# Performance work log

Measured on AMD Instinct MI355X. Metric: run time of the kernel, lower is better.

## Reference

```python
import jax, jax.numpy as jnp
import numpy as np

N, E, F_IN, F_HID, F_OUT, B = 50000, 800000, 128, 128, 128, 64
EPS = 1e-5


def _sage_conv(x, src, dst, w_l, b_l, w_r):
    # PyG SAGEConv (mean aggr): out = lin_l(mean_{j in N(i)} x_j) + lin_r(x_i)
    msg_sum = jax.ops.segment_sum(x[src], dst, num_segments=N)          # [N, F]
    deg = jax.ops.segment_sum(jnp.ones((src.shape[0],), x.dtype), dst, num_segments=N)
    agg = msg_sum / jnp.clip(deg, 1.0)[:, None]
    return agg @ w_l + b_l + x @ w_r


def _batch_norm(x, gamma, beta):
    # PyG BatchNorm (training): biased batch stats over the node dimension
    mu = jnp.mean(x, axis=0)
    var = jnp.mean((x - mu) ** 2, axis=0)
    return (x - mu) * jax.lax.rsqrt(var + EPS) * gamma + beta


def setup_inputs() -> dict:
    key = jax.random.key(0)
    ks = jax.random.split(key, 12)
    x = jax.random.normal(ks[0], (N, F_IN), jnp.float32)
    edge_index = jax.random.randint(ks[1], (2, E), 0, N, jnp.int64 if jax.config.jax_enable_x64 else jnp.int32)
    batch = jnp.sort(jax.random.randint(ks[2], (N,), 0, B))
    s1 = 1.0 / np.sqrt(F_IN)
    s2 = 1.0 / np.sqrt(F_HID)
    return {
        "x": x, "edge_index": edge_index, "batch": batch,
        "w_l1": jax.random.uniform(ks[3], (F_IN, F_HID), jnp.float32, -s1, s1),
        "b_l1": jax.random.uniform(ks[4], (F_HID,), jnp.float32, -s1, s1),
        "w_r1": jax.random.uniform(ks[5], (F_IN, F_HID), jnp.float32, -s1, s1),
        "g1": jnp.ones((F_HID,), jnp.float32),
        "beta1": jnp.zeros((F_HID,), jnp.float32),
        "w_l2": jax.random.uniform(ks[6], (F_HID, F_OUT), jnp.float32, -s2, s2),
        "b_l2": jax.random.uniform(ks[7], (F_OUT,), jnp.float32, -s2, s2),
        "w_r2": jax.random.uniform(ks[8], (F_HID, F_OUT), jnp.float32, -s2, s2),
        "g2": jnp.ones((F_OUT,), jnp.float32),
        "beta2": jnp.zeros((F_OUT,), jnp.float32),
    }


def reference(x, edge_index, batch, w_l1, b_l1, w_r1, g1, beta1, w_l2, b_l2, w_r2, g2, beta2):
    src, dst = edge_index[0], edge_index[1]
    h = jax.nn.relu(_batch_norm(_sage_conv(x, src, dst, w_l1, b_l1, w_r1), g1, beta1))
    h = jax.nn.relu(_batch_norm(_sage_conv(h, src, dst, w_l2, b_l2, w_r2), g2, beta2))
    # global_mean_pool over graph ids
    pooled = jax.ops.segment_sum(h, batch, num_segments=B)              # [B, F_OUT]
    cnt = jax.ops.segment_sum(jnp.ones((N,), h.dtype), batch, num_segments=B)
    return pooled / jnp.clip(cnt, 1.0)[:, None]
```

## Files before the change

kernel.cpp:

```cpp
#include <hip/hip_runtime.h>
#include <hip/hip_bf16.h>
#include <stdint.h>

typedef unsigned int uint32;
typedef unsigned short ushort16;

typedef __attribute__((ext_vector_type(8))) short short8;
typedef __attribute__((ext_vector_type(4))) float f32x4;

#define N_NODES 50000
#define N_EDGES 800000
#define FD      128
#define NGRAPH  64
#define MTILES  3125
#define NBK     196
#define GB      391
#define GB2     782
#define PCH     32
#define KCH     98

__device__ __forceinline__ float bf2f(ushort16 u){
  union { uint32 i; float f; } v; v.i = ((uint32)u) << 16; return v.f;
}
__device__ __forceinline__ float bf2f_lo(uint32 w){ union{uint32 i;float f;}v; v.i = w << 16; return v.f; }
__device__ __forceinline__ float bf2f_hi(uint32 w){ union{uint32 i;float f;}v; v.i = w & 0xffff0000u; return v.f; }
__device__ __forceinline__ ushort16 f2bf(float f){
  uint32 u = __float_as_uint(f);
  u += 0x7fffu + ((u >> 16) & 1u);
  return (ushort16)(u >> 16);
}

__device__ __forceinline__ int ld_idx(const void* p, uint32 is64, size_t i){
  return is64 ? (int)((const long long*)p)[i] : ((const int*)p)[i];
}
__device__ __forceinline__ float ld_f(const void* p, uint32 isf32, int i){
  return isf32 ? ((const float*)p)[i] : bf2f(((const ushort16*)p)[i]);
}

__device__ __forceinline__ void get_flags(const uint32* __restrict__ xw,
    const uint32* __restrict__ eiw, uint32& isf32, uint32& is64)
{
  int l = threadIdx.x & 63;
  uint32 w = xw[l];
  uint32 e8 = (w >> 7) & 0xFFu;
  bool bf_like = (e8 >= 0x70u && e8 <= 0x82u);
  unsigned long long m = __ballot(bf_like);
  isf32 = (__popcll(m) < 32) ? 1u : 0u;
  uint32 hi = (l < 8) ? eiw[2*l + 1] : 1u;
  unsigned long long z = __ballot(hi == 0u);
  is64 = ((z & 0xFFull) == 0xFFull) ? 1u : 0u;
}


__global__ __launch_bounds__(256) void pack_gseg_prep_kernel(
    const void* __restrict__ ei, const void* __restrict__ batch,
    const void* __restrict__ X,
    const void* __restrict__ WL1, const void* __restrict__ WR1,
    const void* __restrict__ WL2, const void* __restrict__ WR2,
    uint32* __restrict__ pack0, uint32* __restrict__ hist, uint32* __restrict__ gstart,
    ushort16* __restrict__ xb, short* __restrict__ wfrag)
{
  uint32 isf32, is64;
  get_flags((const uint32*)X, (const uint32*)ei, isf32, is64);
  int tid = threadIdx.x;
  if (blockIdx.x < GB){
    __shared__ uint32 h[256];
    h[tid] = 0u;
    __syncthreads();
    int base = blockIdx.x*2048;
    for (int r = 0; r < 8; ++r){
      int i = base + r*256 + tid;
      if (i < N_EDGES){
        uint32 s = (uint32)ld_idx(ei, is64, i);
        uint32 d = (uint32)ld_idx(ei, is64, (size_t)N_EDGES + i);
        pack0[i] = (d << 16) | s;
        atomicAdd(&h[d >> 8], 1u);
      }
    }
    __syncthreads();
    hist[blockIdx.x*256 + tid] = h[tid];
  } else if (blockIdx.x < GB + 196){
    int t = (blockIdx.x - GB)*256 + tid;
    if (t >= N_NODES) return;
    int b1 = ld_idx(batch, is64, t);
    int b0 = (t == 0) ? -1 : ld_idx(batch, is64, t - 1);
    for (int g = b0 + 1; g <= b1; ++g) gstart[g] = (uint32)t;
    if (t == N_NODES - 1)
      for (int g = b1 + 1; g <= NGRAPH; ++g) gstart[g] = (uint32)N_NODES;
  } else if (blockIdx.x < GB + 196 + 3125){
    if (!isf32) return;
    size_t e = ((size_t)(blockIdx.x - GB - 196)*256 + tid)*8;
    const float* p = (const float*)X + e;
    float4 u = *(const float4*)p;
    float4 v = *(const float4*)(p + 4);
    uint4 o;
    o.x = (uint32)f2bf(u.x) | ((uint32)f2bf(u.y) << 16);
    o.y = (uint32)f2bf(u.z) | ((uint32)f2bf(u.w) << 16);
    o.z = (uint32)f2bf(v.x) | ((uint32)f2bf(v.y) << 16);
    o.w = (uint32)f2bf(v.z) | ((uint32)f2bf(v.w) << 16);
    *(uint4*)(xb + e) = o;
  } else {
    int t = (blockIdx.x - GB - 196 - 3125)*256 + tid;
    int layer = t >> 15;
    int r = t & 32767;
    int k = r >> 7, n = r & 127;
    const void* w = layer ? (k < 128 ? WL2 : WR2) : (k < 128 ? WL1 : WR1);
    int kk = k & 127;
    float wv = ld_f(w, isf32, kk*128 + n);
    int off = (((k >> 5)*8 + (n >> 4))*64 + (n & 15) + 16*((kk >> 3) & 3))*8 + (kk & 7);
    wfrag[layer*32768 + off] = (short)f2bf(wv);
  }
}

__global__ __launch_bounds__(1024) void scan_hist_kernel(const uint32* __restrict__ hist,
    uint32* __restrict__ off, uint32* __restrict__ bbase)
{
  __shared__ uint32 part[4][256];
  __shared__ uint32 lds[256];
  __shared__ uint32 bb[256];
  int tid = threadIdx.x;
  int seg = tid >> 8, b = tid & 255;
  int k0 = seg*KCH, k1 = (k0 + KCH < GB) ? k0 + KCH : GB;
  uint32 sum = 0;
  for (int k = k0; k < k1; ++k) sum += hist[k*256 + b];
  part[seg][b] = sum;
  __syncthreads();
  uint32 tot = 0, x = 0;
  if (seg == 0){
    tot = part[0][b] + part[1][b] + part[2][b] + part[3][b];
    x = tot; lds[b] = x;
  }
  __syncthreads();
  for (int o = 1; o < 256; o <<= 1){
    uint32 y = 0;
    if (seg == 0 && b >= o) y = lds[b - o];
    __syncthreads();
    if (seg == 0){ x += y; lds[b] = x; }
    __syncthreads();
  }
  if (seg == 0){
    uint32 base = x - tot;
    bb[b] = base;
    if (b <= NBK) bbase[b] = (b < NBK) ? base : (uint32)N_EDGES;
  }
  __syncthreads();
  uint32 run = bb[b];
  for (int s = 0; s < seg; ++s) run += part[s][b];
  for (int k = k0; k < k1; ++k){
    off[k*256 + b] = run;
    run += hist[k*256 + b];
  }
}

__global__ __launch_bounds__(256) void scatter_kernel(const uint32* __restrict__ pack0,
    const uint32* __restrict__ off, uint32* __restrict__ pack1)
{
  __shared__ uint32 cur[256];
  int tid = threadIdx.x;
  cur[tid] = off[blockIdx.x*256 + tid];
  __syncthreads();
  int base = blockIdx.x*2048;
  for (int r = 0; r < 8; ++r){
    int i = base + r*256 + tid;
    if (i < N_EDGES){
      uint32 p = pack0[i];
      uint32 pos = atomicAdd(&cur[p >> 24], 1u);
      pack1[pos] = p;
    }
  }
}

__global__ __launch_bounds__(256) void bucket_csr_kernel(const uint32* __restrict__ pack1,
    const uint32* __restrict__ bbase, uint32* __restrict__ rowstart,
    uint32* __restrict__ deg, ushort16* __restrict__ colidx, uint32* __restrict__ perm)
{
  __shared__ uint32 cnt[256];
  __shared__ uint32 lds[256];
  __shared__ uint32 cur[256];
  __shared__ uint32 dh[64];
  __shared__ uint32 dcur[64];
  int tid = threadIdx.x;
  int bk = blockIdx.x;
  uint32 e0 = bbase[bk], e1 = bbase[bk + 1];
  cnt[tid] = 0u;
  if (tid < 64) dh[tid] = 0u;
  __syncthreads();
  for (uint32 i = e0 + tid; i < e1; i += 256)
    atomicAdd(&cnt[(pack1[i] >> 16) & 255u], 1u);
  __syncthreads();
  uint32 v = cnt[tid];
  uint32 x = v;
  lds[tid] = x; __syncthreads();
  for (int o = 1; o < 256; o <<= 1){
    uint32 y = (tid >= o) ? lds[tid - o] : 0u;
    __syncthreads();
    x += y; lds[tid] = x;
    __syncthreads();
  }
  uint32 start = e0 + x - v;
  int node = bk*256 + tid;
  bool nvalid = node < N_NODES;
  if (nvalid){ rowstart[node] = start; deg[node] = v; }
  cur[tid] = start;
  uint32 bin = (v < 63u) ? v : 63u;
  if (nvalid) atomicAdd(&dh[bin], 1u);
  __syncthreads();
  for (uint32 i = e0 + tid; i < e1; i += 256){
    uint32 p = pack1[i];
    uint32 pos = atomicAdd(&cur[(p >> 16) & 255u], 1u);
    colidx[pos] = (ushort16)(p & 0xFFFFu);
  }
  if (tid == 0){
    uint32 run = 0;
#pragma unroll
    for (int b2 = 0; b2 < 64; ++b2){ dcur[b2] = run; run += dh[b2]; }
  }
  __syncthreads();
  if (nvalid){
    uint32 rank = atomicAdd(&dcur[bin], 1u);
    perm[bk*256 + rank] = (uint32)node;
  }
}


__device__ __forceinline__ void acc8(float* a, uint4 v, const float* s0, const float* h0, int APPLY){
  float f[8];
  f[0] = bf2f_lo(v.x); f[1] = bf2f_hi(v.x);
  f[2] = bf2f_lo(v.y); f[3] = bf2f_hi(v.y);
  f[4] = bf2f_lo(v.z); f[5] = bf2f_hi(v.z);
  f[6] = bf2f_lo(v.w); f[7] = bf2f_hi(v.w);
#pragma unroll
  for (int j = 0; j < 8; ++j)
    a[j] += APPLY ? fmaxf(f[j]*s0[j] + h0[j], 0.f) : f[j];
}

template<int APPLY>
__global__ __launch_bounds__(256) void agg_kernel(const ushort16* __restrict__ Xd,
    const void* __restrict__ Xraw, const void* __restrict__ eiraw,
    const uint32* __restrict__ rowstart, const uint32* __restrict__ deg,
    const ushort16* __restrict__ colidx, const uint32* __restrict__ perm,
    const float* __restrict__ sc, const float* __restrict__ sh,
    ushort16* __restrict__ out)
{
  uint32 isf32, is64;
  get_flags((const uint32*)Xraw, (const uint32*)eiraw, isf32, is64);
  const ushort16* X = (APPLY == 0 && !isf32) ? (const ushort16*)Xraw : Xd;
  int t = blockIdx.x*256 + threadIdx.x;
  int node = (int)perm[t >> 4];
  int l = t & 15;
  uint32 st = rowstart[node];
  uint32 d  = deg[node];
  float s0[8], h0[8];
#pragma unroll
  for (int j = 0; j < 8; ++j){
    s0[j] = APPLY ? sc[l*8 + j] : 0.f;
    h0[j] = APPLY ? sh[l*8 + j] : 0.f;
  }
  float a[8];
#pragma unroll
  for (int j = 0; j < 8; ++j) a[j] = 0.f;
  const ushort16* Xl = X + l*8;
  uint32 i = 0;
  for (; i < d && ((st + i) & 3u); ++i){
    uint32 c = colidx[st + i];
    acc8(a, *(const uint4*)(Xl + (size_t)c*FD), s0, h0, APPLY);
  }
  for (; i + 8 <= d; i += 8){
    uint2 cA = *(const uint2*)(colidx + st + i);
    uint2 cB = *(const uint2*)(colidx + st + i + 4);
    uint4 v0 = *(const uint4*)(Xl + (size_t)(cA.x & 0xFFFFu)*FD);
    uint4 v1 = *(const uint4*)(Xl + (size_t)(cA.x >> 16)*FD);
    uint4 v2 = *(const uint4*)(Xl + (size_t)(cA.y & 0xFFFFu)*FD);
    uint4 v3 = *(const uint4*)(Xl + (size_t)(cA.y >> 16)*FD);
    uint4 v4 = *(const uint4*)(Xl + (size_t)(cB.x & 0xFFFFu)*FD);
    uint4 v5 = *(const uint4*)(Xl + (size_t)(cB.x >> 16)*FD);
    uint4 v6 = *(const uint4*)(Xl + (size_t)(cB.y & 0xFFFFu)*FD);
    uint4 v7 = *(const uint4*)(Xl + (size_t)(cB.y >> 16)*FD);
    acc8(a, v0, s0, h0, APPLY); acc8(a, v1, s0, h0, APPLY);
    acc8(a, v2, s0, h0, APPLY); acc8(a, v3, s0, h0, APPLY);
    acc8(a, v4, s0, h0, APPLY); acc8(a, v5, s0, h0, APPLY);
    acc8(a, v6, s0, h0, APPLY); acc8(a, v7, s0, h0, APPLY);
  }
  for (; i + 4 <= d; i += 4){
    uint2 cA = *(const uint2*)(colidx + st + i);
    uint4 v0 = *(const uint4*)(Xl + (size_t)(cA.x & 0xFFFFu)*FD);
    uint4 v1 = *(const uint4*)(Xl + (size_t)(cA.x >> 16)*FD);
    uint4 v2 = *(const uint4*)(Xl + (size_t)(cA.y & 0xFFFFu)*FD);
    uint4 v3 = *(const uint4*)(Xl + (size_t)(cA.y >> 16)*FD);
    acc8(a, v0, s0, h0, APPLY); acc8(a, v1, s0, h0, APPLY);
    acc8(a, v2, s0, h0, APPLY); acc8(a, v3, s0, h0, APPLY);
  }
  for (; i < d; ++i){
    uint32 c = colidx[st + i];
    acc8(a, *(const uint4*)(Xl + (size_t)c*FD), s0, h0, APPLY);
  }
  float inv = 1.f / fmaxf((float)d, 1.f);
  uint4 o;
  o.x = (uint32)f2bf(a[0]*inv) | ((uint32)f2bf(a[1]*inv) << 16);
  o.y = (uint32)f2bf(a[2]*inv) | ((uint32)f2bf(a[3]*inv) << 16);
  o.z = (uint32)f2bf(a[4]*inv) | ((uint32)f2bf(a[5]*inv) << 16);
  o.w = (uint32)f2bf(a[6]*inv) | ((uint32)f2bf(a[7]*inv) << 16);
  *(uint4*)(out + (size_t)node*FD + l*8) = o;
}


__device__ __forceinline__ short8 affine_relu8(short8 a, const float* sc, const float* sh, int koff){
  short8 r;
#pragma unroll
  for (int j = 0; j < 8; ++j){
    float v = bf2f((ushort16)a[j]) * sc[koff + j] + sh[koff + j];
    r[j] = (short)f2bf(fmaxf(v, 0.f));
  }
  return r;
}

template<int APPLY>
__global__ __launch_bounds__(256) void gemm_bn_kernel(
    const ushort16* __restrict__ A0, const ushort16* __restrict__ A1d,
    const void* __restrict__ A1raw, const void* __restrict__ eiraw,
    const short* __restrict__ wfrag, const void* __restrict__ bias,
    const float* __restrict__ sc, const float* __restrict__ sh,
    const void* __restrict__ Xraw,
    ushort16* __restrict__ hpre, float* __restrict__ bnpart)
{
  __shared__ float red[256];
  uint32 isf32, is64;
  get_flags((const uint32*)Xraw, (const uint32*)eiraw, isf32, is64);
  const ushort16* A1 = (A1raw && !isf32) ? (const ushort16*)A1raw : A1d;
  int tid = threadIdx.x;
  red[tid] = 0.f;
  int wave = tid >> 6, lane = tid & 63, lq = lane >> 4, lm = lane & 15;
  int mt = blockIdx.x*4 + wave;
  bool valid = mt < MTILES;
  size_t m0 = (size_t)((valid ? mt : 0)*16 + lm);
  f32x4 acc[8];
#pragma unroll
  for (int i = 0; i < 8; ++i) acc[i] = (f32x4){0.f,0.f,0.f,0.f};

#pragma unroll
  for (int ks = 0; ks < 8; ++ks){
    int koff = (ks & 3)*32 + lq*8;
    const short* srcp = (const short*)(ks < 4 ? A0 : A1);
    short8 a = *(const short8*)(srcp + m0*FD + koff);
    if (APPLY && ks >= 4) a = affine_relu8(a, sc, sh, koff);
#pragma unroll
    for (int nt = 0; nt < 8; ++nt){
      short8 b = *(const short8*)&wfrag[((ks*8 + nt)*64 + lane)*8];
      acc[nt] = __builtin_amdgcn_mfma_f32_16x16x32_bf16(a, b, acc[nt], 0, 0, 0);
    }
  }

  __syncthreads();
#pragma unroll
  for (int nt = 0; nt < 8; ++nt){
    int colc = nt*16 + lm;
    float bb = ld_f(bias, isf32, colc);
    float s = 0.f, s2 = 0.f;
    if (valid){
      size_t nb = (size_t)mt*16 + lq*4;
#pragma unroll
      for (int r = 0; r < 4; ++r){
        float val = acc[nt][r] + bb;
        hpre[(nb + r)*FD + colc] = f2bf(val);
        s += val; s2 += val*val;
      }
    }
    s  += __shfl_xor(s, 16);  s  += __shfl_xor(s, 32);
    s2 += __shfl_xor(s2, 16); s2 += __shfl_xor(s2, 32);
    if (lq == 0){
      atomicAdd(&red[colc], s);
      atomicAdd(&red[128 + colc], s2);
    }
  }
  __syncthreads();
  bnpart[blockIdx.x*256 + tid] = red[tid];
}


__global__ __launch_bounds__(256) void bn_final_kernel(const float* __restrict__ bnpart,
    const void* __restrict__ gamma, const void* __restrict__ beta,
    const void* __restrict__ Xraw, const void* __restrict__ eiraw,
    float* __restrict__ scale, float* __restrict__ shift)
{
  uint32 isf32, is64;
  get_flags((const uint32*)Xraw, (const uint32*)eiraw, isf32, is64);
  int tid = threadIdx.x;
  int f = blockIdx.x*8 + (tid >> 5);
  int l = tid & 31;
  float s = 0.f, q = 0.f;
  for (int b = l; b < GB2; b += 32){
    s += bnpart[b*256 + f];
    q += bnpart[b*256 + 128 + f];
  }
#pragma unroll
  for (int m = 16; m >= 1; m >>= 1){
    s += __shfl_xor(s, m);
    q += __shfl_xor(q, m);
  }
  if (l == 0){
    const float invN = 1.0f / (float)N_NODES;
    float mu  = s * invN;
    float var = q * invN - mu*mu;
    float scv = ld_f(gamma, isf32, f) * rsqrtf(var + 1e-5f);
    scale[f] = scv;
    shift[f] = ld_f(beta, isf32, f) - mu * scv;
  }
}


__global__ __launch_bounds__(256) void pool_partial_kernel(const ushort16* __restrict__ hp,
    const float* __restrict__ scale, const float* __restrict__ shift,
    const uint32* __restrict__ gstart, float* __restrict__ pool_part)
{
  __shared__ float wred[4*16*8];
  int tid = threadIdx.x;
  int g = blockIdx.x >> 5, chunk = blockIdx.x & 31;
  int slot = tid >> 4, l = tid & 15;
  int wave = tid >> 6, lane = tid & 63;
  uint32 st = gstart[g], cnt = gstart[g+1] - st;
  uint32 per = (cnt + PCH - 1) >> 5;
  uint32 b0 = st + chunk*per;
  uint32 b1 = b0 + per;
  uint32 e1 = st + cnt;
  if (b1 > e1) b1 = e1;
  float s0[8], h0[8], a[8];
#pragma unroll
  for (int j = 0; j < 8; ++j){ s0[j] = scale[l*8 + j]; h0[j] = shift[l*8 + j]; a[j] = 0.f; }
  for (uint32 n = b0 + slot; n < b1; n += 16){
    const uint4 v = *(const uint4*)(hp + (size_t)n*FD + l*8);
    float f[8];
    f[0] = bf2f_lo(v.x); f[1] = bf2f_hi(v.x);
    f[2] = bf2f_lo(v.y); f[3] = bf2f_hi(v.y);
    f[4] = bf2f_lo(v.z); f[5] = bf2f_hi(v.z);
    f[6] = bf2f_lo(v.w); f[7] = bf2f_hi(v.w);
#pragma unroll
    for (int j = 0; j < 8; ++j) a[j] += fmaxf(f[j]*s0[j] + h0[j], 0.f);
  }
#pragma unroll
  for (int j = 0; j < 8; ++j){
    a[j] += __shfl_xor(a[j], 16);
    a[j] += __shfl_xor(a[j], 32);
  }
  if (lane < 16){
#pragma unroll
    for (int j = 0; j < 8; ++j) wred[(wave*16 + lane)*8 + j] = a[j];
  }
  __syncthreads();
  if (tid < 16){
    float r[8];
#pragma unroll
    for (int j = 0; j < 8; ++j)
      r[j] = wred[(0*16 + tid)*8 + j] + wred[(1*16 + tid)*8 + j]
           + wred[(2*16 + tid)*8 + j] + wred[(3*16 + tid)*8 + j];
    float* dst = pool_part + (size_t)blockIdx.x*FD + tid*8;
#pragma unroll
    for (int j = 0; j < 8; ++j) dst[j] = r[j];
  }
}

__global__ void pool_final_kernel(const float* __restrict__ pool_part,
    const uint32* __restrict__ gstart, const void* __restrict__ Xraw,
    const void* __restrict__ eiraw, void* __restrict__ out)
{
  uint32 isf32, is64;
  get_flags((const uint32*)Xraw, (const uint32*)eiraw, isf32, is64);
  int t = blockIdx.x*256 + threadIdx.x;
  int g = t >> 7, f = t & 127;
  float c = fmaxf((float)(gstart[g+1] - gstart[g]), 1.f);
  float v = 0.f;
#pragma unroll 8
  for (int ch = 0; ch < PCH; ++ch)
    v += pool_part[(size_t)(g*PCH + ch)*FD + f];
  v /= c;
  if (isf32) ((float*)out)[t] = v;
  else       ((ushort16*)out)[t] = f2bf(v);
}


extern "C" void kernel_launch(void* const* d_in, const int* in_sizes, int n_in,
                              void* d_out, int out_size, void* d_ws, size_t ws_size,
                              hipStream_t stream)
{
  const void* x   = d_in[0];
  const void* ei  = d_in[1];
  const void* bat = d_in[2];
  const void* wl1 = d_in[3];
  const void* bl1 = d_in[4];
  const void* wr1 = d_in[5];
  const void* g1  = d_in[6];
  const void* be1 = d_in[7];
  const void* wl2 = d_in[8];
  const void* bl2 = d_in[9];
  const void* wr2 = d_in[10];
  const void* g2  = d_in[11];
  const void* be2 = d_in[12];
  char* ws = (char*)d_ws;

  uint32* gstart  = (uint32*)(ws + 64);
  uint32* bbase   = (uint32*)(ws + 384);
  float*  scale1  = (float*) (ws + 1280);
  float*  shift1  = (float*) (ws + 1792);
  float*  scale2  = (float*) (ws + 2304);
  float*  shift2  = (float*) (ws + 2816);
  uint32* rowstart= (uint32*)(ws + 3328);
  uint32* deg     = (uint32*)(ws + 203328);
  ushort16* colidx= (ushort16*)(ws + 403328);
  uint32* perm    = (uint32*)(ws + 2003328);
  short*  wfrag   = (short*) (ws + 2204032);
  float*  bnpart  = (float*) (ws + 2335104);
  ushort16* xb    = (ushort16*)(ws + 3135872);
  ushort16* aggb  = (ushort16*)(ws + 15935872);
  ushort16* hp1   = (ushort16*)(ws + 28735872);
  ushort16* hp2   = (ushort16*)(ws + 41535872);
  uint32* pack0   = (uint32*)(ws + 28735872);
  uint32* pack1   = (uint32*)(ws + 31935872);
  uint32* hist    = (uint32*)(ws + 35135872);
  uint32* off     = (uint32*)(ws + 35536256);
  float*  ppart   = (float*) (ws + 28735872);

  pack_gseg_prep_kernel<<<GB + 196 + 3125 + 256, 256, 0, stream>>>(
      ei, bat, x, wl1, wr1, wl2, wr2, pack0, hist, gstart, xb, wfrag);
  scan_hist_kernel <<<1,  1024, 0, stream>>>(hist, off, bbase);
  scatter_kernel   <<<GB,  256, 0, stream>>>(pack0, off, pack1);
  bucket_csr_kernel<<<NBK, 256, 0, stream>>>(pack1, bbase, rowstart, deg, colidx, perm);

  agg_kernel<0>    <<<3125, 256, 0, stream>>>(xb, x, ei, rowstart, deg, colidx, perm,
                                              nullptr, nullptr, aggb);
  gemm_bn_kernel<0><<<GB2,  256, 0, stream>>>(aggb, xb, x, ei, wfrag, bl1,
                                              nullptr, nullptr, x, hp1, bnpart);
  bn_final_kernel  <<<16,   256, 0, stream>>>(bnpart, g1, be1, x, ei, scale1, shift1);

  agg_kernel<1>    <<<3125, 256, 0, stream>>>(hp1, x, ei, rowstart, deg, colidx, perm,
                                              scale1, shift1, aggb);
  gemm_bn_kernel<1><<<GB2,  256, 0, stream>>>(aggb, hp1, nullptr, ei, wfrag + 32768, bl2,
                                              scale1, shift1, x, hp2, bnpart);
  bn_final_kernel  <<<16,   256, 0, stream>>>(bnpart, g2, be2, x, ei, scale2, shift2);

  pool_partial_kernel<<<NGRAPH*PCH, 256, 0, stream>>>(hp2, scale2, shift2, gstart, ppart);
  pool_final_kernel  <<<32,  256, 0, stream>>>(ppart, gstart, x, ei, d_out);
}
```

Baseline: 297.1 us.

## Split histogram scan into three parallel kernels and drop degree-sorted node permutation

The single-block 1024-thread prefix scan over the edge bucket histogram is replaced by a three-stage scan: partial sums over 16 blocks, a single-block middle scan, and a 16-block offset write. This spreads the serial column walk across more compute units at the cost of two extra launches. Separately, the per-bucket degree-sorting permutation is removed, so the aggregation kernels process nodes in natural order. That saves the perm build and the indirection load, but gives up degree-balanced wavefronts, which may increase divergence in the gather loops.

```diff
diff --git a/kernel.cpp b/kernel.cpp
--- a/kernel.cpp
+++ b/kernel.cpp
@@ -17,7 +17,8 @@
 #define GB      391
 #define GB2     782
 #define PCH     32
-#define KCH     98
+#define SBK     16
+#define KCH2    25
 
 __device__ __forceinline__ float bf2f(ushort16 u){
   union { uint32 i; float f; } v; v.i = ((uint32)u) << 16; return v.f;
@@ -112,40 +113,49 @@
   }
 }
 
-__global__ __launch_bounds__(1024) void scan_hist_kernel(const uint32* __restrict__ hist,
-    uint32* __restrict__ off, uint32* __restrict__ bbase)
-{
-  __shared__ uint32 part[4][256];
-  __shared__ uint32 lds[256];
-  __shared__ uint32 bb[256];
-  int tid = threadIdx.x;
-  int seg = tid >> 8, b = tid & 255;
-  int k0 = seg*KCH, k1 = (k0 + KCH < GB) ? k0 + KCH : GB;
+
+__global__ __launch_bounds__(256) void scan_part_kernel(const uint32* __restrict__ hist,
+    uint32* __restrict__ part)
+{
+  int b = threadIdx.x, p = blockIdx.x;
+  int k0 = p*KCH2, k1 = (k0 + KCH2 < GB) ? k0 + KCH2 : GB;
   uint32 sum = 0;
   for (int k = k0; k < k1; ++k) sum += hist[k*256 + b];
-  part[seg][b] = sum;
-  __syncthreads();
-  uint32 tot = 0, x = 0;
-  if (seg == 0){
-    tot = part[0][b] + part[1][b] + part[2][b] + part[3][b];
-    x = tot; lds[b] = x;
-  }
-  __syncthreads();
+  part[p*256 + b] = sum;
+}
+
+__global__ __launch_bounds__(256) void scan_mid_kernel(const uint32* __restrict__ part,
+    uint32* __restrict__ pbase, uint32* __restrict__ bbase)
+{
+  __shared__ uint32 lds[256];
+  int b = threadIdx.x;
+  uint32 tot = 0;
+#pragma unroll
+  for (int p = 0; p < SBK; ++p) tot += part[p*256 + b];
+  uint32 x = tot;
+  lds[b] = x; __syncthreads();
   for (int o = 1; o < 256; o <<= 1){
-    uint32 y = 0;
-    if (seg == 0 && b >= o) y = lds[b - o];
+    uint32 y = (b >= o) ? lds[b - o] : 0u;
     __syncthreads();
-    if (seg == 0){ x += y; lds[b] = x; }
+    x += y; lds[b] = x;
     __syncthreads();
   }
-  if (seg == 0){
-    uint32 base = x - tot;
-    bb[b] = base;
-    if (b <= NBK) bbase[b] = (b < NBK) ? base : (uint32)N_EDGES;
-  }
-  __syncthreads();
-  uint32 run = bb[b];
-  for (int s = 0; s < seg; ++s) run += part[s][b];
+  uint32 base = x - tot;
+  if (b <= NBK) bbase[b] = (b < NBK) ? base : (uint32)N_EDGES;
+  uint32 run = base;
+#pragma unroll
+  for (int p = 0; p < SBK; ++p){
+    pbase[p*256 + b] = run;
+    run += part[p*256 + b];
+  }
+}
+
+__global__ __launch_bounds__(256) void scan_off_kernel(const uint32* __restrict__ hist,
+    const uint32* __restrict__ pbase, uint32* __restrict__ off)
+{
+  int b = threadIdx.x, p = blockIdx.x;
+  int k0 = p*KCH2, k1 = (k0 + KCH2 < GB) ? k0 + KCH2 : GB;
+  uint32 run = pbase[p*256 + b];
   for (int k = k0; k < k1; ++k){
     off[k*256 + b] = run;
     run += hist[k*256 + b];
@@ -172,18 +182,15 @@
 
 __global__ __launch_bounds__(256) void bucket_csr_kernel(const uint32* __restrict__ pack1,
     const uint32* __restrict__ bbase, uint32* __restrict__ rowstart,
-    uint32* __restrict__ deg, ushort16* __restrict__ colidx, uint32* __restrict__ perm)
+    uint32* __restrict__ deg, ushort16* __restrict__ colidx)
 {
   __shared__ uint32 cnt[256];
   __shared__ uint32 lds[256];
   __shared__ uint32 cur[256];
-  __shared__ uint32 dh[64];
-  __shared__ uint32 dcur[64];
   int tid = threadIdx.x;
   int bk = blockIdx.x;
   uint32 e0 = bbase[bk], e1 = bbase[bk + 1];
   cnt[tid] = 0u;
-  if (tid < 64) dh[tid] = 0u;
   __syncthreads();
   for (uint32 i = e0 + tid; i < e1; i += 256)
     atomicAdd(&cnt[(pack1[i] >> 16) & 255u], 1u);
@@ -199,26 +206,13 @@
   }
   uint32 start = e0 + x - v;
   int node = bk*256 + tid;
-  bool nvalid = node < N_NODES;
-  if (nvalid){ rowstart[node] = start; deg[node] = v; }
+  if (node < N_NODES){ rowstart[node] = start; deg[node] = v; }
   cur[tid] = start;
-  uint32 bin = (v < 63u) ? v : 63u;
-  if (nvalid) atomicAdd(&dh[bin], 1u);
   __syncthreads();
   for (uint32 i = e0 + tid; i < e1; i += 256){
     uint32 p = pack1[i];
     uint32 pos = atomicAdd(&cur[(p >> 16) & 255u], 1u);
     colidx[pos] = (ushort16)(p & 0xFFFFu);
-  }
-  if (tid == 0){
-    uint32 run = 0;
-#pragma unroll
-    for (int b2 = 0; b2 < 64; ++b2){ dcur[b2] = run; run += dh[b2]; }
-  }
-  __syncthreads();
-  if (nvalid){
-    uint32 rank = atomicAdd(&dcur[bin], 1u);
-    perm[bk*256 + rank] = (uint32)node;
   }
 }
 
@@ -238,7 +232,7 @@
 __global__ __launch_bounds__(256) void agg_kernel(const ushort16* __restrict__ Xd,
     const void* __restrict__ Xraw, const void* __restrict__ eiraw,
     const uint32* __restrict__ rowstart, const uint32* __restrict__ deg,
-    const ushort16* __restrict__ colidx, const uint32* __restrict__ perm,
+    const ushort16* __restrict__ colidx,
     const float* __restrict__ sc, const float* __restrict__ sh,
     ushort16* __restrict__ out)
 {
@@ -246,7 +240,7 @@
   get_flags((const uint32*)Xraw, (const uint32*)eiraw, isf32, is64);
   const ushort16* X = (APPLY == 0 && !isf32) ? (const ushort16*)Xraw : Xd;
   int t = blockIdx.x*256 + threadIdx.x;
-  int node = (int)perm[t >> 4];
+  int node = t >> 4;
   int l = t & 15;
   uint32 st = rowstart[node];
   uint32 d  = deg[node];
@@ -505,7 +499,8 @@
   uint32* rowstart= (uint32*)(ws + 3328);
   uint32* deg     = (uint32*)(ws + 203328);
   ushort16* colidx= (ushort16*)(ws + 403328);
-  uint32* perm    = (uint32*)(ws + 2003328);
+  uint32* part    = (uint32*)(ws + 2003328);
+  uint32* pbase   = (uint32*)(ws + 2019712);
   short*  wfrag   = (short*) (ws + 2204032);
   float*  bnpart  = (float*) (ws + 2335104);
   ushort16* xb    = (ushort16*)(ws + 3135872);
@@ -520,17 +515,19 @@
 
   pack_gseg_prep_kernel<<<GB + 196 + 3125 + 256, 256, 0, stream>>>(
       ei, bat, x, wl1, wr1, wl2, wr2, pack0, hist, gstart, xb, wfrag);
-  scan_hist_kernel <<<1,  1024, 0, stream>>>(hist, off, bbase);
+  scan_part_kernel <<<SBK, 256, 0, stream>>>(hist, part);
+  scan_mid_kernel  <<<1,   256, 0, stream>>>(part, pbase, bbase);
+  scan_off_kernel  <<<SBK, 256, 0, stream>>>(hist, pbase, off);
   scatter_kernel   <<<GB,  256, 0, stream>>>(pack0, off, pack1);
-  bucket_csr_kernel<<<NBK, 256, 0, stream>>>(pack1, bbase, rowstart, deg, colidx, perm);
-
-  agg_kernel<0>    <<<3125, 256, 0, stream>>>(xb, x, ei, rowstart, deg, colidx, perm,
+  bucket_csr_kernel<<<NBK, 256, 0, stream>>>(pack1, bbase, rowstart, deg, colidx);
+
+  agg_kernel<0>    <<<3125, 256, 0, stream>>>(xb, x, ei, rowstart, deg, colidx,
                                               nullptr, nullptr, aggb);
   gemm_bn_kernel<0><<<GB2,  256, 0, stream>>>(aggb, xb, x, ei, wfrag, bl1,
                                               nullptr, nullptr, x, hp1, bnpart);
   bn_final_kernel  <<<16,   256, 0, stream>>>(bnpart, g1, be1, x, ei, scale1, shift1);
 
-  agg_kernel<1>    <<<3125, 256, 0, stream>>>(hp1, x, ei, rowstart, deg, colidx, perm,
+  agg_kernel<1>    <<<3125, 256, 0, stream>>>(hp1, x, ei, rowstart, deg, colidx,
                                               scale1, shift1, aggb);
   gemm_bn_kernel<1><<<GB2,  256, 0, stream>>>(aggb, hp1, nullptr, ei, wfrag + 32768, bl2,
                                               scale1, shift1, x, hp2, bnpart);
```

Result: faster. 269.3 us (-9.4%).
